# Performance work log

Measured on AMD Instinct MI355X. Metric: run time of the kernel, lower is better.

The kernel has to match this reference:

```python
import jax, jax.numpy as jnp
import numpy as np


def setup_inputs() -> dict:
    key = jax.random.key(0)
    k1, k2, k3, k4, k5 = jax.random.split(key, 5)
    B, K, S, E, I, D = 4, 2, 512, 8, 1024, 2048
    x = jax.random.normal(k1, (B, S, I), dtype=jnp.float32)
    weights = jax.random.uniform(k2, (B, K, S), dtype=jnp.float32)
    ensembles = jax.random.randint(k3, (B, K, S), 0, E, dtype=jnp.int64)
    # xavier_uniform-style init for expert weight tables
    lim1 = float(np.sqrt(6.0 / (D + I)))
    proj_in = jax.random.uniform(k4, (E, D, I), dtype=jnp.float32, minval=-lim1, maxval=lim1)
    proj_out = jax.random.uniform(k5, (E, I, D), dtype=jnp.float32, minval=-lim1, maxval=lim1)
    return {"x": x, "weights": weights, "ensembles": ensembles,
            "proj_in": proj_in, "proj_out": proj_out}


def reference(x, weights, ensembles, proj_in, proj_out):
    # x: (B,S,I); weights/ensembles: (B,K,S); proj_in: (E,D,I); proj_out: (E,I,D)
    # Same math as the torch module (dropout = identity in eval):
    #   per token t, out = sum_k w[k,t] * W2[e_kt] @ relu(W1[e_kt] @ x[t])
    # Computed as all-expert batched GEMMs + a gated (one-hot scatter) combine,
    # which is mathematically identical and avoids the (B,K,S,D,I) gather blowup.
    E = proj_in.shape[0]
    h = jax.nn.relu(jnp.einsum('edi,bsi->bsed', proj_in, x))      # (B,S,E,D)
    o = jnp.einsum('eid,bsed->bsei', proj_out, h)                 # (B,S,E,I)
    onehot = jax.nn.one_hot(ensembles, E, dtype=x.dtype)          # (B,K,S,E)
    gate = jnp.einsum('bks,bkse->bse', weights, onehot)           # (B,S,E)
    return jnp.einsum('bsei,bse->bsi', o, gate)                   # (B,S,I)
```

## Files before the change

kernel.cpp:

```cpp
#include <hip/hip_runtime.h>
#include <stdint.h>

#define THREADS 512
#define NE 8
#define BB 4
#define SS 512
#define KK 2
#define II 1024
#define DD 2048
#define NTOK (BB * SS)
#define NASSIGN (BB * KK * SS)

#define F4_X (NTOK * II / 4)
#define F4_P (NE * DD * II / 4)
#define CVB_X (F4_X / 1024)
#define CVB_P (F4_P / 1024)
#define CVB_TOTAL (CVB_X + 2 * CVB_P)

typedef unsigned short u16;
typedef __attribute__((ext_vector_type(8))) __bf16 bf16x8;
typedef __attribute__((ext_vector_type(4))) float f32x4;
typedef __attribute__((ext_vector_type(4))) unsigned int u32x4;

__device__ __forceinline__ u16 f32_to_bf16(float f) {
    unsigned int u = __builtin_bit_cast(unsigned int, f);
    unsigned int r = u + 0x7FFFu + ((u >> 16) & 1u);
    return (u16)(r >> 16);
}

__device__ __forceinline__ unsigned int pk2(float a, float b) {
    return (unsigned int)f32_to_bf16(a) | ((unsigned int)f32_to_bf16(b) << 16);
}

__device__ __forceinline__ void gload16(const void* g, void* l) {
    __builtin_amdgcn_global_load_lds(
        (const __attribute__((address_space(1))) unsigned int*)g,
        (__attribute__((address_space(3))) unsigned int*)l, 16, 0, 0);
}

#define BARRIER() do { \
    __builtin_amdgcn_sched_barrier(0); \
    __builtin_amdgcn_s_barrier(); \
    __builtin_amdgcn_sched_barrier(0); } while (0)

__device__ void setup_body(const void* __restrict__ ens_raw,
                           const float* __restrict__ weights,
                           int* __restrict__ meta,
                           int* __restrict__ tok,
                           float* __restrict__ wgt) {
    __shared__ int s_cnt[NE];
    __shared__ int s_cur[NE];
    __shared__ int s_flag;
    const int t = threadIdx.x;
    if (t < NE) s_cnt[t] = 0;
    if (t == 0) s_flag = 0;
    __syncthreads();

    const unsigned int* w32 = (const unsigned int*)ens_raw;
    unsigned int f = 0;
    for (int i = t; i < NASSIGN / 2; i += 256) f |= w32[2 * i + 1];
    if (f) atomicOr(&s_flag, 1);
    __syncthreads();
    const bool is32 = (s_flag != 0);
    const int* e32 = (const int*)ens_raw;
    const long long* e64 = (const long long*)ens_raw;

    for (int a = t; a < NASSIGN; a += 256) {
        int e = is32 ? e32[a] : (int)e64[a];
        atomicAdd(&s_cnt[e & 7], 1);
    }
    __syncthreads();

    if (t == 0) {
        int pb = 0, nt = 0;
        for (int e = 0; e < NE; e++) {
            int c = s_cnt[e];
            meta[8 + e] = c;
            meta[16 + e] = pb;
            s_cur[e] = pb;
            int n128 = (c + 127) >> 7;
            int pe = pb + n128 * 128;
            for (int i2 = 0; i2 < n128; i2 += 2) {
                meta[32 + nt] = e;
                meta[64 + nt] = pb + i2 * 128;
                meta[96 + nt] = pb + c;
                meta[128 + nt] = pe;
                nt++;
            }
            pb = pe;
        }
        meta[0] = nt;
        meta[1] = pb;
    }
    __syncthreads();

    for (int a = t; a < NASSIGN; a += 256) {
        int e = is32 ? e32[a] : (int)e64[a];
        e &= 7;
        int slot = atomicAdd(&s_cur[e], 1);
        int b = a >> 10;
        int s = a & (SS - 1);
        tok[slot] = b * SS + s;
        wgt[slot] = weights[a];
    }
    __syncthreads();

    for (int e = 0; e < NE; e++) {
        int st = meta[16 + e] + meta[8 + e];
        int en = (e < NE - 1) ? meta[16 + e + 1] : meta[1];
        for (int i = st + t; i < en; i += 256) {
            tok[i] = 0;
            wgt[i] = 0.f;
        }
    }
}

__global__ __launch_bounds__(256)
void convert_setup(const float* __restrict__ x,
                   const float* __restrict__ pin,
                   const float* __restrict__ pout,
                   u16* __restrict__ xb,
                   u16* __restrict__ pb1,
                   u16* __restrict__ pb2,
                   const void* __restrict__ ens,
                   const float* __restrict__ weights,
                   int* __restrict__ meta,
                   int* __restrict__ tok,
                   float* __restrict__ wgt) {
    const int b = blockIdx.x;
    if (b >= CVB_TOTAL) {
        setup_body(ens, weights, meta, tok, wgt);
        return;
    }
    const float* s;
    u16* d;
    size_t base;
    if (b < CVB_X)             { s = x;    d = xb;  base = (size_t)b * 1024; }
    else if (b < CVB_X + CVB_P){ s = pin;  d = pb1; base = (size_t)(b - CVB_X) * 1024; }
    else                       { s = pout; d = pb2; base = (size_t)(b - CVB_X - CVB_P) * 1024; }
    const f32x4* s4 = (const f32x4*)s;
    f32x4 v[4];
#pragma unroll
    for (int q = 0; q < 4; q++)
        v[q] = __builtin_nontemporal_load(&s4[base + q * 256 + threadIdx.x]);
#pragma unroll
    for (int q = 0; q < 4; q++) {
        uint2 o;
        o.x = pk2(v[q][0], v[q][1]);
        o.y = pk2(v[q][2], v[q][3]);
        *(uint2*)(d + 4 * (base + q * 256 + threadIdx.x)) = o;
    }
}

__global__ __launch_bounds__(THREADS, 2)
void gemm1(const u16* __restrict__ Abase,
           const u16* __restrict__ Bbase,
           const int* __restrict__ meta,
           const int* __restrict__ tok,
           u16* __restrict__ hdst) {
    constexpr int NT = II / 64;
    constexpr int ASZ = 256 * 64 * 2;
    constexpr int BUFSZ = 2 * ASZ;
    __shared__ char smem[2 * BUFSZ];

    const int lid = blockIdx.x;
    const int g = lid & 7;
    const int i = lid >> 3;
    const int tile = g + 8 * (i % 3);
    const int colt = i / 3;
    if (tile >= meta[0]) return;

    const int e     = meta[32 + tile];
    const int sbase = meta[64 + tile];
    const int wend  = meta[128 + tile];
    const int padmax = meta[1];
    const int colbase = colt * 256;

    const int tid = threadIdx.x;
    const int lane = tid & 63;
    const int wv = tid >> 6;
    const int wr = wv >> 2;
    const int wc = wv & 3;

    const u16* Bp = Bbase + (size_t)e * (size_t)(DD * II) + (size_t)colbase * II;

    int aoff[4], boff[4], cdst[4];
#pragma unroll
    for (int j = 0; j < 4; j++) {
        int c = j * 512 + tid;
        int row = c >> 3;
        int s = (c & 7) ^ (row & 7);
        cdst[j] = c * 16;
        int slot = sbase + row;
        if (slot > padmax - 1) slot = padmax - 1;
        aoff[j] = tok[slot] * II + s * 8;
        boff[j] = row * II + s * 8;
    }

    f32x4 acc[8][4];
#pragma unroll
    for (int m = 0; m < 8; m++)
#pragma unroll
        for (int n = 0; n < 4; n++)
            acc[m][n] = (f32x4){0.f, 0.f, 0.f, 0.f};

    auto STAGE = [&](int kt, char* buf) {
        const int kof = kt * 64;
#pragma unroll
        for (int j = 0; j < 4; j++)
            gload16(Abase + aoff[j] + kof, buf + cdst[j]);
#pragma unroll
        for (int j = 0; j < 4; j++)
            gload16(Bp + boff[j] + kof, buf + ASZ + cdst[j]);
    };

    auto COMPUTE = [&](const char* buf) {
        const u16* As = (const u16*)buf;
        const u16* Bs = (const u16*)(buf + ASZ);
#pragma unroll
        for (int kk = 0; kk < 2; kk++) {
            bf16x8 a[8], b[4];
#pragma unroll
            for (int m = 0; m < 8; m++) {
                int row = wr * 128 + m * 16 + (lane & 15);
                int slot = (kk * 4 + (lane >> 4)) ^ (row & 7);
                a[m] = *(const bf16x8*)&As[row * 64 + slot * 8];
            }
#pragma unroll
            for (int n = 0; n < 4; n++) {
                int col = wc * 64 + n * 16 + (lane & 15);
                int slot = (kk * 4 + (lane >> 4)) ^ (col & 7);
                b[n] = *(const bf16x8*)&Bs[col * 64 + slot * 8];
            }
            asm volatile("s_waitcnt lgkmcnt(0)" ::: "memory");
            __builtin_amdgcn_sched_barrier(0);
            __builtin_amdgcn_s_setprio(1);
#pragma unroll
            for (int m = 0; m < 8; m++)
#pragma unroll
                for (int n = 0; n < 4; n++)
                    acc[m][n] = __builtin_amdgcn_mfma_f32_16x16x32_bf16(
                        a[m], b[n], acc[m][n], 0, 0, 0);
            __builtin_amdgcn_s_setprio(0);
        }
    };

    char* buf0 = smem;
    char* buf1 = smem + BUFSZ;

    STAGE(0, buf0);
    asm volatile("s_waitcnt vmcnt(0)" ::: "memory");
    BARRIER();

#pragma unroll 1
    for (int t = 0; t < NT; ++t) {
        char* cur = (t & 1) ? buf1 : buf0;
        char* nxt = (t & 1) ? buf0 : buf1;
        const bool st = (t + 1 < NT);
        if (st) STAGE(t + 1, nxt);
        COMPUTE(cur);
        if (st) asm volatile("s_waitcnt vmcnt(0)" ::: "memory");
        BARRIER();
    }

#pragma unroll
    for (int m = 0; m < 8; m++) {
#pragma unroll
        for (int r = 0; r < 4; r++) {
            int row = wr * 128 + m * 16 + (lane >> 4) * 4 + r;
            int slot = sbase + row;
            if (slot < wend) {
                size_t ro = (size_t)slot * DD;
#pragma unroll
                for (int n = 0; n < 4; n++) {
                    int col = colbase + wc * 64 + n * 16 + (lane & 15);
                    float v = acc[m][n][r];
                    v = v > 0.f ? v : 0.f;
                    hdst[ro + col] = f32_to_bf16(v);
                }
            }
        }
    }
}

__global__ __launch_bounds__(THREADS, 2)
void gemm2(const u16* __restrict__ Abase,
           const u16* __restrict__ Bbase,
           const int* __restrict__ meta,
           const int* __restrict__ tok,
           const float* __restrict__ wgt,
           float* __restrict__ outdst) {
    constexpr int NT = DD / 64;
    constexpr int ASZ = 256 * 64 * 2;
    constexpr int BSZ = 128 * 64 * 2;
    constexpr int BUFSZ = ASZ + BSZ;
    __shared__ char smem[3 * BUFSZ];

    const int lid = blockIdx.x;
    const int g = lid & 7;
    const int i = lid >> 3;
    const int tile = g + 8 * (i % 3);
    const int colt = i / 3;
    if (tile >= meta[0]) return;

    const int e     = meta[32 + tile];
    const int sbase = meta[64 + tile];
    const int rend  = meta[96 + tile];
    const int padmax = meta[1];
    const int colbase = colt * 128;

    const int tid = threadIdx.x;
    const int lane = tid & 63;
    const int wv = tid >> 6;
    const int wr = wv >> 1;
    const int wc = wv & 1;

    const u16* Bp = Bbase + (size_t)e * (size_t)(DD * II) + (size_t)colbase * DD;

    int aoff[4], adst[4], boff[2], bdst[2];
#pragma unroll
    for (int j = 0; j < 4; j++) {
        int c = j * 512 + tid;
        int row = c >> 3;
        int s = (c & 7) ^ (row & 7);
        adst[j] = c * 16;
        int slot = sbase + row;
        if (slot > padmax - 1) slot = padmax - 1;
        aoff[j] = slot * DD + s * 8;
    }
#pragma unroll
    for (int j = 0; j < 2; j++) {
        int c = j * 512 + tid;
        int row = c >> 3;
        int s = (c & 7) ^ (row & 7);
        bdst[j] = c * 16;
        boff[j] = row * DD + s * 8;
    }

    f32x4 acc[4][4];
#pragma unroll
    for (int m = 0; m < 4; m++)
#pragma unroll
        for (int n = 0; n < 4; n++)
            acc[m][n] = (f32x4){0.f, 0.f, 0.f, 0.f};

    auto STAGE = [&](int kt, char* buf) {
        const int kof = kt * 64;
#pragma unroll
        for (int j = 0; j < 4; j++)
            gload16(Abase + aoff[j] + kof, buf + adst[j]);
#pragma unroll
        for (int j = 0; j < 2; j++)
            gload16(Bp + boff[j] + kof, buf + ASZ + bdst[j]);
    };

    auto COMPUTE = [&](const char* buf) {
        const u16* As = (const u16*)buf;
        const u16* Bs = (const u16*)(buf + ASZ);
        bf16x8 a[2][4], b[2][4];
#pragma unroll
        for (int kk = 0; kk < 2; kk++) {
#pragma unroll
            for (int m = 0; m < 4; m++) {
                int row = wr * 64 + m * 16 + (lane & 15);
                int slot = (kk * 4 + (lane >> 4)) ^ (row & 7);
                a[kk][m] = *(const bf16x8*)&As[row * 64 + slot * 8];
            }
#pragma unroll
            for (int n = 0; n < 4; n++) {
                int col = wc * 64 + n * 16 + (lane & 15);
                int slot = (kk * 4 + (lane >> 4)) ^ (col & 7);
                b[kk][n] = *(const bf16x8*)&Bs[col * 64 + slot * 8];
            }
        }
        asm volatile("s_waitcnt lgkmcnt(0)" ::: "memory");
        __builtin_amdgcn_sched_barrier(0);
        __builtin_amdgcn_s_setprio(1);
#pragma unroll
        for (int m = 0; m < 4; m++)
#pragma unroll
            for (int n = 0; n < 4; n++) {
                acc[m][n] = __builtin_amdgcn_mfma_f32_16x16x32_bf16(
                    a[0][m], b[0][n], acc[m][n], 0, 0, 0);
                acc[m][n] = __builtin_amdgcn_mfma_f32_16x16x32_bf16(
                    a[1][m], b[1][n], acc[m][n], 0, 0, 0);
            }
        __builtin_amdgcn_s_setprio(0);
    };

    char* pA = smem;
    char* pB = smem + BUFSZ;
    char* pC = smem + 2 * BUFSZ;

    STAGE(0, pA);
    STAGE(1, pB);
    asm volatile("s_waitcnt vmcnt(6)" ::: "memory");
    BARRIER();

#pragma unroll 1
    for (int t = 0; t < NT; ++t) {
        const bool st = (t + 2 < NT);
        if (st) STAGE(t + 2, pC);
        COMPUTE(pA);
        if (st) {
            asm volatile("s_waitcnt vmcnt(6)" ::: "memory");
        } else if (t + 1 < NT) {
            asm volatile("s_waitcnt vmcnt(0)" ::: "memory");
        }
        BARRIER();
        { char* tp = pA; pA = pB; pB = pC; pC = tp; }
    }

#pragma unroll
    for (int m = 0; m < 4; m++) {
#pragma unroll
        for (int r = 0; r < 4; r++) {
            int row = wr * 64 + m * 16 + (lane >> 4) * 4 + r;
            int slot = sbase + row;
            if (slot < rend) {
                float w = wgt[slot];
                size_t obase = (size_t)tok[slot] * II;
#pragma unroll
                for (int n = 0; n < 4; n++) {
                    int col = colbase + wc * 64 + n * 16 + (lane & 15);
                    atomicAdd(&outdst[obase + col], acc[m][n][r] * w);
                }
            }
        }
    }
}

extern "C" void kernel_launch(void* const* d_in, const int* in_sizes, int n_in,
                              void* d_out, int out_size, void* d_ws, size_t ws_size,
                              hipStream_t stream) {
    const float* x = (const float*)d_in[0];
    const float* weights = (const float*)d_in[1];
    const void* ens = d_in[2];
    const float* pin = (const float*)d_in[3];
    const float* pout = (const float*)d_in[4];
    float* out = (float*)d_out;

    char* ws = (char*)d_ws;
    int*   meta    = (int*)(ws);
    int*   tok     = (int*)(ws + 1024);
    float* wgt     = (float*)(ws + 21504);
    u16*   x_bf    = (u16*)(ws + 41984);
    u16*   pin_bf  = (u16*)(ws + 4236288);
    u16*   pout_bf = (u16*)(ws + 37790720);
    u16*   h       = (u16*)(ws + 71345152);

    hipMemsetAsync(d_out, 0, (size_t)out_size * sizeof(float), stream);

    convert_setup<<<dim3(CVB_TOTAL + 1), dim3(256), 0, stream>>>(
        x, pin, pout, x_bf, pin_bf, pout_bf, ens, weights, meta, tok, wgt);

    gemm1<<<dim3(8 * 3 * 8), dim3(THREADS), 0, stream>>>(
        x_bf, pin_bf, meta, tok, h);

    gemm2<<<dim3(8 * 3 * 8), dim3(THREADS), 0, stream>>>(
        h, pout_bf, meta, tok, wgt, out);
}
```

Baseline: 126.1 us.

## Split-K gemm2 with 256x256 tiles, separate setup kernel, wider convert chunks

After: 142.3 us. 12.9% more time.

```diff
diff --git a/kernel.cpp b/kernel.cpp
--- a/kernel.cpp
+++ b/kernel.cpp
@@ -11,11 +11,11 @@
 #define NTOK (BB * SS)
 #define NASSIGN (BB * KK * SS)
 
-#define F4_X (NTOK * II / 4)
-#define F4_P (NE * DD * II / 4)
-#define CVB_X (F4_X / 1024)
-#define CVB_P (F4_P / 1024)
-#define CVB_TOTAL (CVB_X + 2 * CVB_P)
+#define CH_X (NTOK * II / 8)
+#define CH_P (NE * DD * II / 8)
+#define CB_X (CH_X / 256)
+#define CB_P (CH_P / 256)
+#define CB_TOTAL (CB_X + 2 * CB_P)
 
 typedef unsigned short u16;
 typedef __attribute__((ext_vector_type(8))) __bf16 bf16x8;
@@ -28,10 +28,6 @@
     return (u16)(r >> 16);
 }
 
-__device__ __forceinline__ unsigned int pk2(float a, float b) {
-    return (unsigned int)f32_to_bf16(a) | ((unsigned int)f32_to_bf16(b) << 16);
-}
-
 __device__ __forceinline__ void gload16(const void* g, void* l) {
     __builtin_amdgcn_global_load_lds(
         (const __attribute__((address_space(1))) unsigned int*)g,
@@ -43,11 +39,11 @@
     __builtin_amdgcn_s_barrier(); \
     __builtin_amdgcn_sched_barrier(0); } while (0)
 
-__device__ void setup_body(const void* __restrict__ ens_raw,
-                           const float* __restrict__ weights,
-                           int* __restrict__ meta,
-                           int* __restrict__ tok,
-                           float* __restrict__ wgt) {
+__global__ void setup_kernel(const void* __restrict__ ens_raw,
+                             const float* __restrict__ weights,
+                             int* __restrict__ meta,
+                             int* __restrict__ tok,
+                             float* __restrict__ wgt) {
     __shared__ int s_cnt[NE];
     __shared__ int s_cur[NE];
     __shared__ int s_flag;
@@ -116,40 +112,29 @@
 }
 
 __global__ __launch_bounds__(256)
-void convert_setup(const float* __restrict__ x,
-                   const float* __restrict__ pin,
-                   const float* __restrict__ pout,
-                   u16* __restrict__ xb,
-                   u16* __restrict__ pb1,
-                   u16* __restrict__ pb2,
-                   const void* __restrict__ ens,
-                   const float* __restrict__ weights,
-                   int* __restrict__ meta,
-                   int* __restrict__ tok,
-                   float* __restrict__ wgt) {
+void convert3(const float* __restrict__ x,
+              const float* __restrict__ pin,
+              const float* __restrict__ pout,
+              u16* __restrict__ xb,
+              u16* __restrict__ pb1,
+              u16* __restrict__ pb2) {
     const int b = blockIdx.x;
-    if (b >= CVB_TOTAL) {
-        setup_body(ens, weights, meta, tok, wgt);
-        return;
-    }
     const float* s;
     u16* d;
-    size_t base;
-    if (b < CVB_X)             { s = x;    d = xb;  base = (size_t)b * 1024; }
-    else if (b < CVB_X + CVB_P){ s = pin;  d = pb1; base = (size_t)(b - CVB_X) * 1024; }
-    else                       { s = pout; d = pb2; base = (size_t)(b - CVB_X - CVB_P) * 1024; }
+    int base;
+    if (b < CB_X)            { s = x;    d = xb;  base = b << 8; }
+    else if (b < CB_X + CB_P){ s = pin;  d = pb1; base = (b - CB_X) << 8; }
+    else                     { s = pout; d = pb2; base = (b - CB_X - CB_P) << 8; }
+    const size_t k = (size_t)base + threadIdx.x;
     const f32x4* s4 = (const f32x4*)s;
-    f32x4 v[4];
-#pragma unroll
-    for (int q = 0; q < 4; q++)
-        v[q] = __builtin_nontemporal_load(&s4[base + q * 256 + threadIdx.x]);
-#pragma unroll
-    for (int q = 0; q < 4; q++) {
-        uint2 o;
-        o.x = pk2(v[q][0], v[q][1]);
-        o.y = pk2(v[q][2], v[q][3]);
-        *(uint2*)(d + 4 * (base + q * 256 + threadIdx.x)) = o;
-    }
+    f32x4 a = __builtin_nontemporal_load(&s4[2 * k]);
+    f32x4 c = __builtin_nontemporal_load(&s4[2 * k + 1]);
+    union { u16 u[8]; u32x4 v; } o;
+    o.u[0] = f32_to_bf16(a[0]); o.u[1] = f32_to_bf16(a[1]);
+    o.u[2] = f32_to_bf16(a[2]); o.u[3] = f32_to_bf16(a[3]);
+    o.u[4] = f32_to_bf16(c[0]); o.u[5] = f32_to_bf16(c[1]);
+    o.u[6] = f32_to_bf16(c[2]); o.u[7] = f32_to_bf16(c[3]);
+    *(u32x4*)(d + 8 * k) = o.v;
 }
 
 __global__ __launch_bounds__(THREADS, 2)
@@ -290,56 +275,51 @@
            const int* __restrict__ tok,
            const float* __restrict__ wgt,
            float* __restrict__ outdst) {
-    constexpr int NT = DD / 64;
+    constexpr int NT = 16;
     constexpr int ASZ = 256 * 64 * 2;
-    constexpr int BSZ = 128 * 64 * 2;
-    constexpr int BUFSZ = ASZ + BSZ;
-    __shared__ char smem[3 * BUFSZ];
+    constexpr int BUFSZ = 2 * ASZ;
+    __shared__ char smem[2 * BUFSZ];
 
     const int lid = blockIdx.x;
     const int g = lid & 7;
     const int i = lid >> 3;
     const int tile = g + 8 * (i % 3);
-    const int colt = i / 3;
+    const int rest = i / 3;
+    const int colt = rest & 3;
+    const int ks = rest >> 2;
     if (tile >= meta[0]) return;
 
     const int e     = meta[32 + tile];
     const int sbase = meta[64 + tile];
     const int rend  = meta[96 + tile];
     const int padmax = meta[1];
-    const int colbase = colt * 128;
+    const int colbase = colt * 256;
+    const int kbase = ks * 1024;
 
     const int tid = threadIdx.x;
     const int lane = tid & 63;
     const int wv = tid >> 6;
-    const int wr = wv >> 1;
-    const int wc = wv & 1;
+    const int wr = wv >> 2;
+    const int wc = wv & 3;
 
     const u16* Bp = Bbase + (size_t)e * (size_t)(DD * II) + (size_t)colbase * DD;
 
-    int aoff[4], adst[4], boff[2], bdst[2];
+    int aoff[4], boff[4], cdst[4];
 #pragma unroll
     for (int j = 0; j < 4; j++) {
         int c = j * 512 + tid;
         int row = c >> 3;
         int s = (c & 7) ^ (row & 7);
-        adst[j] = c * 16;
+        cdst[j] = c * 16;
         int slot = sbase + row;
         if (slot > padmax - 1) slot = padmax - 1;
-        aoff[j] = slot * DD + s * 8;
-    }
-#pragma unroll
-    for (int j = 0; j < 2; j++) {
-        int c = j * 512 + tid;
-        int row = c >> 3;
-        int s = (c & 7) ^ (row & 7);
-        bdst[j] = c * 16;
-        boff[j] = row * DD + s * 8;
-    }
-
-    f32x4 acc[4][4];
-#pragma unroll
-    for (int m = 0; m < 4; m++)
+        aoff[j] = slot * DD + kbase + s * 8;
+        boff[j] = row * DD + kbase + s * 8;
+    }
+
+    f32x4 acc[8][4];
+#pragma unroll
+    for (int m = 0; m < 8; m++)
 #pragma unroll
         for (int n = 0; n < 4; n++)
             acc[m][n] = (f32x4){0.f, 0.f, 0.f, 0.f};
@@ -348,74 +328,66 @@
         const int kof = kt * 64;
 #pragma unroll
         for (int j = 0; j < 4; j++)
-            gload16(Abase + aoff[j] + kof, buf + adst[j]);
-#pragma unroll
-        for (int j = 0; j < 2; j++)
-            gload16(Bp + boff[j] + kof, buf + ASZ + bdst[j]);
+            gload16(Abase + aoff[j] + kof, buf + cdst[j]);
+#pragma unroll
+        for (int j = 0; j < 4; j++)
+            gload16(Bp + boff[j] + kof, buf + ASZ + cdst[j]);
     };
 
     auto COMPUTE = [&](const char* buf) {
         const u16* As = (const u16*)buf;
         const u16* Bs = (const u16*)(buf + ASZ);
-        bf16x8 a[2][4], b[2][4];
 #pragma unroll
         for (int kk = 0; kk < 2; kk++) {
-#pragma unroll
-            for (int m = 0; m < 4; m++) {
-                int row = wr * 64 + m * 16 + (lane & 15);
+            bf16x8 a[8], b[4];
+#pragma unroll
+            for (int m = 0; m < 8; m++) {
+                int row = wr * 128 + m * 16 + (lane & 15);
                 int slot = (kk * 4 + (lane >> 4)) ^ (row & 7);
-                a[kk][m] = *(const bf16x8*)&As[row * 64 + slot * 8];
+                a[m] = *(const bf16x8*)&As[row * 64 + slot * 8];
             }
 #pragma unroll
             for (int n = 0; n < 4; n++) {
                 int col = wc * 64 + n * 16 + (lane & 15);
                 int slot = (kk * 4 + (lane >> 4)) ^ (col & 7);
-                b[kk][n] = *(const bf16x8*)&Bs[col * 64 + slot * 8];
-            }
-        }
-        asm volatile("s_waitcnt lgkmcnt(0)" ::: "memory");
-        __builtin_amdgcn_sched_barrier(0);
-        __builtin_amdgcn_s_setprio(1);
-#pragma unroll
-        for (int m = 0; m < 4; m++)
-#pragma unroll
-            for (int n = 0; n < 4; n++) {
-                acc[m][n] = __builtin_amdgcn_mfma_f32_16x16x32_bf16(
-                    a[0][m], b[0][n], acc[m][n], 0, 0, 0);
-                acc[m][n] = __builtin_amdgcn_mfma_f32_16x16x32_bf16(
-                    a[1][m], b[1][n], acc[m][n], 0, 0, 0);
-            }
-        __builtin_amdgcn_s_setprio(0);
+                b[n] = *(const bf16x8*)&Bs[col * 64 + slot * 8];
+            }
+            asm volatile("s_waitcnt lgkmcnt(0)" ::: "memory");
+            __builtin_amdgcn_sched_barrier(0);
+            __builtin_amdgcn_s_setprio(1);
+#pragma unroll
+            for (int m = 0; m < 8; m++)
+#pragma unroll
+                for (int n = 0; n < 4; n++)
+                    acc[m][n] = __builtin_amdgcn_mfma_f32_16x16x32_bf16(
+                        a[m], b[n], acc[m][n], 0, 0, 0);
+            __builtin_amdgcn_s_setprio(0);
+        }
     };
 
-    char* pA = smem;
-    char* pB = smem + BUFSZ;
-    char* pC = smem + 2 * BUFSZ;
-
-    STAGE(0, pA);
-    STAGE(1, pB);
-    asm volatile("s_waitcnt vmcnt(6)" ::: "memory");
+    char* buf0 = smem;
+    char* buf1 = smem + BUFSZ;
+
+    STAGE(0, buf0);
+    asm volatile("s_waitcnt vmcnt(0)" ::: "memory");
     BARRIER();
 
 #pragma unroll 1
     for (int t = 0; t < NT; ++t) {
-        const bool st = (t + 2 < NT);
-        if (st) STAGE(t + 2, pC);
-        COMPUTE(pA);
-        if (st) {
-            asm volatile("s_waitcnt vmcnt(6)" ::: "memory");
-        } else if (t + 1 < NT) {
-            asm volatile("s_waitcnt vmcnt(0)" ::: "memory");
-        }
+        char* cur = (t & 1) ? buf1 : buf0;
+        char* nxt = (t & 1) ? buf0 : buf1;
+        const bool st = (t + 1 < NT);
+        if (st) STAGE(t + 1, nxt);
+        COMPUTE(cur);
+        if (st) asm volatile("s_waitcnt vmcnt(0)" ::: "memory");
         BARRIER();
-        { char* tp = pA; pA = pB; pB = pC; pC = tp; }
-    }
-
-#pragma unroll
-    for (int m = 0; m < 4; m++) {
+    }
+
+#pragma unroll
+    for (int m = 0; m < 8; m++) {
 #pragma unroll
         for (int r = 0; r < 4; r++) {
-            int row = wr * 64 + m * 16 + (lane >> 4) * 4 + r;
+            int row = wr * 128 + m * 16 + (lane >> 4) * 4 + r;
             int slot = sbase + row;
             if (slot < rend) {
                 float w = wgt[slot];
@@ -449,10 +421,12 @@
     u16*   pout_bf = (u16*)(ws + 37790720);
     u16*   h       = (u16*)(ws + 71345152);
 
+    setup_kernel<<<dim3(1), dim3(256), 0, stream>>>(ens, weights, meta, tok, wgt);
+
     hipMemsetAsync(d_out, 0, (size_t)out_size * sizeof(float), stream);
 
-    convert_setup<<<dim3(CVB_TOTAL + 1), dim3(256), 0, stream>>>(
-        x, pin, pout, x_bf, pin_bf, pout_bf, ens, weights, meta, tok, wgt);
+    convert3<<<dim3(CB_TOTAL), dim3(256), 0, stream>>>(
+        x, pin, pout, x_bf, pin_bf, pout_bf);
 
     gemm1<<<dim3(8 * 3 * 8), dim3(THREADS), 0, stream>>>(
         x_bf, pin_bf, meta, tok, h);
```
